# Optimization experiments

Measured on AMD Instinct MI355X. Metric: run time of the kernel, lower is better.

Reference implementation:

```python
import jax, jax.numpy as jnp
import numpy as np
from jax.scipy.special import logsumexp

REG = 1.0
N_ITER = 50  # fixed Sinkhorn iterations (log-domain, stabilized)


def setup_inputs() -> dict:
    key = jax.random.key(0)
    k1, k2 = jax.random.split(key)
    source = jax.random.normal(k1, (8192, 256), dtype=jnp.float32)
    target = jax.random.normal(k2, (8192, 256), dtype=jnp.float32)
    return {"source": source, "target": target}


def _sinkhorn_value(x, y, reg):
    # squared euclidean cost matrix [n, m]
    M = (jnp.sum(x * x, axis=1)[:, None]
         + jnp.sum(y * y, axis=1)[None, :]
         - 2.0 * (x @ y.T))
    n, m = M.shape
    loga = -jnp.log(jnp.float32(n))  # uniform weights
    logb = -jnp.log(jnp.float32(m))
    Mr = M / reg

    def step(fg, _):
        f, g = fg
        # f_i = -reg * logsumexp_j((g_j - M_ij)/reg + log b_j)
        f = -reg * logsumexp(g[None, :] / reg - Mr + logb, axis=1)
        g = -reg * logsumexp(f[:, None] / reg - Mr + loga, axis=0)
        return (f, g), None

    f0 = jnp.zeros((n,), dtype=M.dtype)
    g0 = jnp.zeros((m,), dtype=M.dtype)
    (f, g), _ = jax.lax.scan(step, (f0, g0), None, length=N_ITER)

    # log P_ij = (f_i + g_j - M_ij)/reg + log a_i + log b_j
    logP = (f[:, None] + g[None, :]) / reg - Mr + (loga + logb)
    P = jnp.exp(logP)
    value_linear = jnp.sum(P * M)
    # KL(P || a x b) entropic term (reg_type='KL' default in POT)
    kl = jnp.sum(P * (logP - loga - logb))
    return value_linear + reg * kl


def reference(source, target):
    value = _sinkhorn_value(source, target, REG)
    return jnp.sqrt(value)
```

## Files before the change

### kernel.cpp

```cpp
#include <hip/hip_runtime.h>

#define N 8192
#define DK 256
#define LOG2E 1.4426950408889634f
#define LN2   0.6931471805599453f
#define ZS    2.5f
#define QS    1.1541560327f
#define BIAS  320.0f

typedef unsigned short u16;
typedef u16   ushort8 __attribute__((ext_vector_type(8)));
typedef __bf16 bf16x8 __attribute__((ext_vector_type(8)));
typedef float  f32x4  __attribute__((ext_vector_type(4)));

__device__ __forceinline__ u16 f2bf(float f){
  unsigned u = __builtin_bit_cast(unsigned, f);
  return (u16)((u + 0x7fffu + ((u >> 16) & 1u)) >> 16);
}
__device__ __forceinline__ float ex2(float x){
  float r; asm("v_exp_f32 %0, %1" : "=v"(r) : "v"(x)); return r;
}
__device__ __forceinline__ float lg2(float x){
  float r; asm("v_log_f32 %0, %1" : "=v"(r) : "v"(x)); return r;
}
__device__ __forceinline__ float cub0(unsigned u){ float r; asm("v_cvt_f32_ubyte0 %0, %1":"=v"(r):"v"(u)); return r; }
__device__ __forceinline__ float cub1(unsigned u){ float r; asm("v_cvt_f32_ubyte1 %0, %1":"=v"(r):"v"(u)); return r; }
__device__ __forceinline__ float cub2(unsigned u){ float r; asm("v_cvt_f32_ubyte2 %0, %1":"=v"(r):"v"(u)); return r; }
__device__ __forceinline__ float cub3(unsigned u){ float r; asm("v_cvt_f32_ubyte3 %0, %1":"=v"(r):"v"(u)); return r; }

__device__ __forceinline__ float quad(unsigned u, float4 gv, float M){
  float t0 = __builtin_fmaf(cub0(u), ZS, gv.x - M);
  float t1 = __builtin_fmaf(cub1(u), ZS, gv.y - M);
  float t2 = __builtin_fmaf(cub2(u), ZS, gv.z - M);
  float t3 = __builtin_fmaf(cub3(u), ZS, gv.w - M);
  return (ex2(t0) + ex2(t1)) + (ex2(t2) + ex2(t3));
}
__device__ __forceinline__ void upd16(const uint4 a, const float* gp, float& m, float& s){
  const float4 g0 = *(const float4*)(gp);
  const float4 g1 = *(const float4*)(gp + 4);
  const float4 g2 = *(const float4*)(gp + 8);
  const float4 g3 = *(const float4*)(gp + 12);
  float t0  = __builtin_fmaf(cub0(a.x), ZS, g0.x);
  float t1  = __builtin_fmaf(cub1(a.x), ZS, g0.y);
  float t2  = __builtin_fmaf(cub2(a.x), ZS, g0.z);
  float t3  = __builtin_fmaf(cub3(a.x), ZS, g0.w);
  float t4  = __builtin_fmaf(cub0(a.y), ZS, g1.x);
  float t5  = __builtin_fmaf(cub1(a.y), ZS, g1.y);
  float t6  = __builtin_fmaf(cub2(a.y), ZS, g1.z);
  float t7  = __builtin_fmaf(cub3(a.y), ZS, g1.w);
  float t8  = __builtin_fmaf(cub0(a.z), ZS, g2.x);
  float t9  = __builtin_fmaf(cub1(a.z), ZS, g2.y);
  float t10 = __builtin_fmaf(cub2(a.z), ZS, g2.z);
  float t11 = __builtin_fmaf(cub3(a.z), ZS, g2.w);
  float t12 = __builtin_fmaf(cub0(a.w), ZS, g3.x);
  float t13 = __builtin_fmaf(cub1(a.w), ZS, g3.y);
  float t14 = __builtin_fmaf(cub2(a.w), ZS, g3.z);
  float t15 = __builtin_fmaf(cub3(a.w), ZS, g3.w);
  float a0 = fmaxf(t0, t1),   a1 = fmaxf(t2, t3);
  float a2 = fmaxf(t4, t5),   a3 = fmaxf(t6, t7);
  float a4 = fmaxf(t8, t9),   a5 = fmaxf(t10, t11);
  float a6 = fmaxf(t12, t13), a7 = fmaxf(t14, t15);
  float b0 = fmaxf(a0, a1), b1 = fmaxf(a2, a3), b2 = fmaxf(a4, a5), b3 = fmaxf(a6, a7);
  float nm = fmaxf(fmaxf(fmaxf(b0, b1), fmaxf(b2, b3)), m);
  float s0 = ex2(t0 - nm) + ex2(t1 - nm) + ex2(t2 - nm) + ex2(t3 - nm)
           + ex2(t4 - nm) + ex2(t5 - nm) + ex2(t6 - nm) + ex2(t7 - nm);
  float s1 = ex2(t8 - nm) + ex2(t9 - nm) + ex2(t10 - nm) + ex2(t11 - nm)
           + ex2(t12 - nm) + ex2(t13 - nm) + ex2(t14 - nm) + ex2(t15 - nm);
  s = __builtin_fmaf(s, ex2(m - nm), s0 + s1);
  m = nm;
}

__global__ __launch_bounds__(256) void prep_k(const float* __restrict__ x, const float* __restrict__ y,
                                              u16* __restrict__ xb, u16* __restrict__ yb,
                                              float* __restrict__ x2, float* __restrict__ y2,
                                              float* __restrict__ gts){
  const int w = threadIdx.x >> 6, l = threadIdx.x & 63;
  const int r = blockIdx.x * 4 + w;
  const bool isx = r < N;
  const int rr = isx ? r : r - N;
  const float* src = (isx ? x : y) + (size_t)rr * DK;
  float4 v = *(const float4*)(src + l * 4);
  ushort4 bv;
  bv.x = f2bf(v.x); bv.y = f2bf(v.y); bv.z = f2bf(v.z); bv.w = f2bf(v.w);
  *(ushort4*)((isx ? xb : yb) + (size_t)rr * DK + l * 4) = bv;
  float p = v.x*v.x + v.y*v.y + v.z*v.z + v.w*v.w;
  #pragma unroll
  for (int off = 32; off > 0; off >>= 1) p += __shfl_down(p, off);
  if (l == 0){
    if (isx) x2[rr] = p;
    else { y2[rr] = p; gts[rr] = -p * LOG2E - BIAS; }
  }
}

__global__ __launch_bounds__(256) void gemm_k(const u16* __restrict__ xb, const u16* __restrict__ yb,
                                              unsigned char* __restrict__ zq,
                                              unsigned char* __restrict__ zqT){
  __shared__ __align__(16) u16 As[128 * 72];
  __shared__ __align__(16) u16 Bs[128 * 72];
  const int t = threadIdx.x;
  const int w = t >> 6, l = t & 63;
  const int wm = w >> 1, wn = w & 1;
  const int brow = blockIdx.y * 128, bcol = blockIdx.x * 128;
  const int tr = t >> 3, tc = t & 7;
  f32x4 acc[4][4] = {};
  for (int ks = 0; ks < 4; ++ks){
    #pragma unroll
    for (int rr = 0; rr < 4; ++rr){
      const int row = tr + rr * 32;
      *(ushort8*)&As[row * 72 + tc * 8] = *(const ushort8*)&xb[(size_t)(brow + row) * DK + ks * 64 + tc * 8];
      *(ushort8*)&Bs[row * 72 + tc * 8] = *(const ushort8*)&yb[(size_t)(bcol + row) * DK + ks * 64 + tc * 8];
    }
    __syncthreads();
    #pragma unroll
    for (int kk = 0; kk < 2; ++kk){
      bf16x8 av[4], bv[4];
      #pragma unroll
      for (int mi = 0; mi < 4; ++mi){
        const int ar = wm * 64 + mi * 16 + (l & 15);
        av[mi] = __builtin_bit_cast(bf16x8, *(const ushort8*)&As[ar * 72 + kk * 32 + (l >> 4) * 8]);
      }
      #pragma unroll
      for (int ni = 0; ni < 4; ++ni){
        const int br = wn * 64 + ni * 16 + (l & 15);
        bv[ni] = __builtin_bit_cast(bf16x8, *(const ushort8*)&Bs[br * 72 + kk * 32 + (l >> 4) * 8]);
      }
      #pragma unroll
      for (int mi = 0; mi < 4; ++mi)
        #pragma unroll
        for (int ni = 0; ni < 4; ++ni)
          acc[mi][ni] = __builtin_amdgcn_mfma_f32_16x16x32_bf16(av[mi], bv[ni], acc[mi][ni], 0, 0, 0);
    }
    __syncthreads();
  }
  unsigned char* Cs = (unsigned char*)As;
  unsigned char* Ct = (unsigned char*)Bs;
  #pragma unroll
  for (int mi = 0; mi < 4; ++mi){
    const int rowb = wm * 64 + mi * 16 + (l >> 4) * 4;
    #pragma unroll
    for (int ni = 0; ni < 4; ++ni){
      const int col = wn * 64 + ni * 16 + (l & 15);
      unsigned pk = 0;
      #pragma unroll
      for (int rr = 0; rr < 4; ++rr){
        float q = fminf(fmaxf(acc[mi][ni][rr] * QS, -127.f), 127.f);
        unsigned b = (unsigned)((int)__builtin_rintf(q) + 128) & 255u;
        Cs[(rowb + rr) * 128 + col] = (unsigned char)b;
        pk |= b << (8 * rr);
      }
      *(unsigned*)(Ct + col * 144 + rowb) = pk;
    }
  }
  __syncthreads();
  const int trow0 = t >> 3, kseg = t & 7;
  #pragma unroll
  for (int ii = 0; ii < 4; ++ii){
    const int row = trow0 + ii * 32;
    int4 v = *(const int4*)(Cs + row * 128 + kseg * 16);
    *(int4*)(zq + (size_t)(brow + row) * N + bcol + kseg * 16) = v;
    int4 vt = *(const int4*)(Ct + row * 144 + kseg * 16);
    *(int4*)(zqT + (size_t)(bcol + row) * N + brow + kseg * 16) = vt;
  }
}

__global__ __launch_bounds__(256) void sweept_k(const unsigned char* __restrict__ z,
                                                const float* __restrict__ din,
                                                float* __restrict__ dout,
                                                float* __restrict__ pmax_out){
  const int w = threadIdx.x >> 6, l = threadIdx.x & 63;
  const int i = blockIdx.x * 4 + w;
  const unsigned char* zr = z + (size_t)i * N + l * 16;
  float m = -1e30f, s = 0.f;
  #pragma unroll 2
  for (int it = 0; it < 8; ++it){
    const uint4 zA = *(const uint4*)(zr + it * 1024);
    upd16(zA, din + it * 1024 + l * 16, m, s);
  }
  #pragma unroll
  for (int off = 32; off > 0; off >>= 1){
    float om = __shfl_down(m, off);
    float os = __shfl_down(s, off);
    float nm = fmaxf(m, om);
    s = __builtin_fmaf(s, ex2(m - nm), os * ex2(om - nm));
    m = nm;
  }
  if (l == 0){
    float lse2 = m + lg2(s);
    dout[i] = 13.0f - lse2 - BIAS;
    pmax_out[i] = lse2;
  }
}

template<int MODE>
__global__ __launch_bounds__(256) void sweepf_k(const unsigned char* __restrict__ z,
                                                const float* __restrict__ din,
                                                float* __restrict__ dout,
                                                const float* __restrict__ pmax_in,
                                                float* __restrict__ pmax_out,
                                                const float* __restrict__ fprev,
                                                const float* __restrict__ x2,
                                                float* __restrict__ contrib){
  const int w = threadIdx.x >> 6, l = threadIdx.x & 63;
  const int r0 = blockIdx.x * 16 + w * 4;
  const unsigned char* zr = z + (size_t)r0 * N + l * 16;
  const float M0 = pmax_in[r0],     M1 = pmax_in[r0 + 1];
  const float M2 = pmax_in[r0 + 2], M3 = pmax_in[r0 + 3];
  float s0 = 0.f, s1 = 0.f, s2 = 0.f, s3 = 0.f;
  #pragma unroll
  for (int it = 0; it < 8; ++it){
    const uint4 a0 = *(const uint4*)(zr + it * 1024);
    const uint4 a1 = *(const uint4*)(zr + N + it * 1024);
    const uint4 a2 = *(const uint4*)(zr + 2 * N + it * 1024);
    const uint4 a3 = *(const uint4*)(zr + 3 * N + it * 1024);
    const float* gp = din + it * 1024 + l * 16;
    const float4 g0 = *(const float4*)(gp);
    const float4 g1 = *(const float4*)(gp + 4);
    const float4 g2 = *(const float4*)(gp + 8);
    const float4 g3 = *(const float4*)(gp + 12);
    s0 += (quad(a0.x, g0, M0) + quad(a0.y, g1, M0))
        + (quad(a0.z, g2, M0) + quad(a0.w, g3, M0));
    s1 += (quad(a1.x, g0, M1) + quad(a1.y, g1, M1))
        + (quad(a1.z, g2, M1) + quad(a1.w, g3, M1));
    s2 += (quad(a2.x, g0, M2) + quad(a2.y, g1, M2))
        + (quad(a2.z, g2, M2) + quad(a2.w, g3, M2));
    s3 += (quad(a3.x, g0, M3) + quad(a3.y, g1, M3))
        + (quad(a3.z, g2, M3) + quad(a3.w, g3, M3));
  }
  #pragma unroll
  for (int off = 32; off > 0; off >>= 1){
    s0 += __shfl_down(s0, off);
    s1 += __shfl_down(s1, off);
    s2 += __shfl_down(s2, off);
    s3 += __shfl_down(s3, off);
  }
  if (l == 0){
    const float lse0 = M0 + lg2(s0);
    const float lse1 = M1 + lg2(s1);
    const float lse2 = M2 + lg2(s2);
    const float lse3 = M3 + lg2(s3);
    if (MODE == 0){
      dout[r0]     = 13.0f - lse0 - BIAS;
      dout[r0 + 1] = 13.0f - lse1 - BIAS;
      dout[r0 + 2] = 13.0f - lse2 - BIAS;
      dout[r0 + 3] = 13.0f - lse3 - BIAS;
      pmax_out[r0]     = lse0;
      pmax_out[r0 + 1] = lse1;
      pmax_out[r0 + 2] = lse2;
      pmax_out[r0 + 3] = lse3;
    } else {
      const float f0 = fprev[r0] + BIAS;
      const float f1 = fprev[r0 + 1] + BIAS;
      const float f2 = fprev[r0 + 2] + BIAS;
      const float f3 = fprev[r0 + 3] + BIAS;
      contrib[r0]     = (f0 * LN2 + x2[r0])     * ex2(f0 + lse0 - 26.0f);
      contrib[r0 + 1] = (f1 * LN2 + x2[r0 + 1]) * ex2(f1 + lse1 - 26.0f);
      contrib[r0 + 2] = (f2 * LN2 + x2[r0 + 2]) * ex2(f2 + lse2 - 26.0f);
      contrib[r0 + 3] = (f3 * LN2 + x2[r0 + 3]) * ex2(f3 + lse3 - 26.0f);
    }
  }
}

__global__ __launch_bounds__(256) void finish_k(const float* __restrict__ contrib,
                                                const float* __restrict__ gts,
                                                const float* __restrict__ y2,
                                                float* __restrict__ out){
  __shared__ float s1[256], s2[256];
  const int t = threadIdx.x;
  float a = 0.f, b = 0.f;
  for (int j = t; j < N; j += 256){ a += contrib[j]; b += (gts[j] + BIAS) * LN2 + y2[j]; }
  s1[t] = a; s2[t] = b; __syncthreads();
  for (int st = 128; st > 0; st >>= 1){
    if (t < st){ s1[t] += s1[t + st]; s2[t] += s2[t + st]; }
    __syncthreads();
  }
  if (t == 0) out[0] = sqrtf(s1[0] + s2[0] * (1.0f / (float)N));
}

extern "C" void kernel_launch(void* const* d_in, const int* in_sizes, int n_in,
                              void* d_out, int out_size, void* d_ws, size_t ws_size,
                              hipStream_t stream){
  const float* x = (const float*)d_in[0];
  const float* y = (const float*)d_in[1];
  float* out = (float*)d_out;
  char* ws = (char*)d_ws;

  unsigned char* zq  = (unsigned char*)(ws);
  unsigned char* zqT = (unsigned char*)(ws + 67108864);
  u16*   xb      = (u16*)  (ws + 134217728);
  u16*   yb      = (u16*)  (ws + 138412032);
  float* x2      = (float*)(ws + 142606336);
  float* y2      = (float*)(ws + 142639104);
  float* fts     = (float*)(ws + 142671872);
  float* gts     = (float*)(ws + 142704640);
  float* contrib = (float*)(ws + 142737408);
  float* pmaxF   = (float*)(ws + 142770176);
  float* pmaxG   = (float*)(ws + 142802944);

  prep_k<<<4096, 256, 0, stream>>>(x, y, xb, yb, x2, y2, gts);
  gemm_k<<<dim3(64, 64), 256, 0, stream>>>(xb, yb, zq, zqT);
  for (int it = 0; it < 2; ++it){
    sweept_k<<<2048, 256, 0, stream>>>(zq,  gts, fts, pmaxF);
    sweept_k<<<2048, 256, 0, stream>>>(zqT, fts, gts, pmaxG);
  }
  for (int s = 4; s < 100; ++s){
    if ((s & 1) == 0)
      sweepf_k<0><<<512, 256, 0, stream>>>(zq,  gts, fts, pmaxF, pmaxF,
                                           nullptr, nullptr, nullptr);
    else
      sweepf_k<0><<<512, 256, 0, stream>>>(zqT, fts, gts, pmaxG, pmaxG,
                                           nullptr, nullptr, nullptr);
  }
  sweepf_k<1><<<512, 256, 0, stream>>>(zq, gts, nullptr, pmaxF, nullptr,
                                       fts, x2, contrib);
  finish_k<<<1, 256, 0, stream>>>(contrib, gts, y2, out);
}
```

Baseline: 1.827 ms.

## Split sweep rows across four waves and raise grid to 2048 blocks

The fixed-max sweep kernel now gives each block 4 rows, with the 4 waves each covering a quarter of the columns, instead of each wave owning 4 full rows. Partial sums are combined through shared memory, and the grid grows from 512 to 2048 blocks. A launch-bounds occupancy hint is also added. The aim is more waves in flight on the MI355X's many CUs, to hide memory latency on the byte-quantized cost matrix. The cost is an extra block barrier and a shared-memory reduction per block.

```diff
diff --git a/kernel.cpp b/kernel.cpp
--- a/kernel.cpp
+++ b/kernel.cpp
@@ -34,6 +34,11 @@
   float t2 = __builtin_fmaf(cub2(u), ZS, gv.z - M);
   float t3 = __builtin_fmaf(cub3(u), ZS, gv.w - M);
   return (ex2(t0) + ex2(t1)) + (ex2(t2) + ex2(t3));
+}
+__device__ __forceinline__ float pm16(const uint4 a, const float4 g0, const float4 g1,
+                                      const float4 g2, const float4 g3, float M){
+  return (quad(a.x, g0, M) + quad(a.y, g1, M))
+       + (quad(a.z, g2, M) + quad(a.w, g3, M));
 }
 __device__ __forceinline__ void upd16(const uint4 a, const float* gp, float& m, float& s){
   const float4 g0 = *(const float4*)(gp);
@@ -192,39 +197,37 @@
 }
 
 template<int MODE>
-__global__ __launch_bounds__(256) void sweepf_k(const unsigned char* __restrict__ z,
-                                                const float* __restrict__ din,
-                                                float* __restrict__ dout,
-                                                const float* __restrict__ pmax_in,
-                                                float* __restrict__ pmax_out,
-                                                const float* __restrict__ fprev,
-                                                const float* __restrict__ x2,
-                                                float* __restrict__ contrib){
+__global__ __launch_bounds__(256, 6) void sweepf_k(const unsigned char* __restrict__ z,
+                                                   const float* __restrict__ din,
+                                                   float* __restrict__ dout,
+                                                   const float* __restrict__ pmax_in,
+                                                   float* __restrict__ pmax_out,
+                                                   const float* __restrict__ fprev,
+                                                   const float* __restrict__ x2,
+                                                   float* __restrict__ contrib){
+  __shared__ float sB[4][4];
   const int w = threadIdx.x >> 6, l = threadIdx.x & 63;
-  const int r0 = blockIdx.x * 16 + w * 4;
-  const unsigned char* zr = z + (size_t)r0 * N + l * 16;
+  const int r0 = blockIdx.x * 4;
+  const int cbase = w * 2048 + l * 16;
+  const unsigned char* zr = z + (size_t)r0 * N + cbase;
   const float M0 = pmax_in[r0],     M1 = pmax_in[r0 + 1];
   const float M2 = pmax_in[r0 + 2], M3 = pmax_in[r0 + 3];
   float s0 = 0.f, s1 = 0.f, s2 = 0.f, s3 = 0.f;
   #pragma unroll
-  for (int it = 0; it < 8; ++it){
+  for (int it = 0; it < 2; ++it){
     const uint4 a0 = *(const uint4*)(zr + it * 1024);
     const uint4 a1 = *(const uint4*)(zr + N + it * 1024);
     const uint4 a2 = *(const uint4*)(zr + 2 * N + it * 1024);
     const uint4 a3 = *(const uint4*)(zr + 3 * N + it * 1024);
-    const float* gp = din + it * 1024 + l * 16;
+    const float* gp = din + cbase + it * 1024;
     const float4 g0 = *(const float4*)(gp);
     const float4 g1 = *(const float4*)(gp + 4);
     const float4 g2 = *(const float4*)(gp + 8);
     const float4 g3 = *(const float4*)(gp + 12);
-    s0 += (quad(a0.x, g0, M0) + quad(a0.y, g1, M0))
-        + (quad(a0.z, g2, M0) + quad(a0.w, g3, M0));
-    s1 += (quad(a1.x, g0, M1) + quad(a1.y, g1, M1))
-        + (quad(a1.z, g2, M1) + quad(a1.w, g3, M1));
-    s2 += (quad(a2.x, g0, M2) + quad(a2.y, g1, M2))
-        + (quad(a2.z, g2, M2) + quad(a2.w, g3, M2));
-    s3 += (quad(a3.x, g0, M3) + quad(a3.y, g1, M3))
-        + (quad(a3.z, g2, M3) + quad(a3.w, g3, M3));
+    s0 += pm16(a0, g0, g1, g2, g3, M0);
+    s1 += pm16(a1, g0, g1, g2, g3, M1);
+    s2 += pm16(a2, g0, g1, g2, g3, M2);
+    s3 += pm16(a3, g0, g1, g2, g3, M3);
   }
   #pragma unroll
   for (int off = 32; off > 0; off >>= 1){
@@ -234,28 +237,21 @@
     s3 += __shfl_down(s3, off);
   }
   if (l == 0){
-    const float lse0 = M0 + lg2(s0);
-    const float lse1 = M1 + lg2(s1);
-    const float lse2 = M2 + lg2(s2);
-    const float lse3 = M3 + lg2(s3);
+    sB[w][0] = s0; sB[w][1] = s1; sB[w][2] = s2; sB[w][3] = s3;
+  }
+  __syncthreads();
+  if (threadIdx.x < 4){
+    const int j = threadIdx.x;
+    const int row = r0 + j;
+    const float s = (sB[0][j] + sB[1][j]) + (sB[2][j] + sB[3][j]);
+    const float M = pmax_in[row];
+    const float lse = M + lg2(s);
     if (MODE == 0){
-      dout[r0]     = 13.0f - lse0 - BIAS;
-      dout[r0 + 1] = 13.0f - lse1 - BIAS;
-      dout[r0 + 2] = 13.0f - lse2 - BIAS;
-      dout[r0 + 3] = 13.0f - lse3 - BIAS;
-      pmax_out[r0]     = lse0;
-      pmax_out[r0 + 1] = lse1;
-      pmax_out[r0 + 2] = lse2;
-      pmax_out[r0 + 3] = lse3;
+      dout[row] = 13.0f - lse - BIAS;
+      pmax_out[row] = lse;
     } else {
-      const float f0 = fprev[r0] + BIAS;
-      const float f1 = fprev[r0 + 1] + BIAS;
-      const float f2 = fprev[r0 + 2] + BIAS;
-      const float f3 = fprev[r0 + 3] + BIAS;
-      contrib[r0]     = (f0 * LN2 + x2[r0])     * ex2(f0 + lse0 - 26.0f);
-      contrib[r0 + 1] = (f1 * LN2 + x2[r0 + 1]) * ex2(f1 + lse1 - 26.0f);
-      contrib[r0 + 2] = (f2 * LN2 + x2[r0 + 2]) * ex2(f2 + lse2 - 26.0f);
-      contrib[r0 + 3] = (f3 * LN2 + x2[r0 + 3]) * ex2(f3 + lse3 - 26.0f);
+      const float f = fprev[row] + BIAS;
+      contrib[row] = (f * LN2 + x2[row]) * ex2(f + lse - 26.0f);
     }
   }
 }
@@ -304,13 +300,13 @@
   }
   for (int s = 4; s < 100; ++s){
     if ((s & 1) == 0)
-      sweepf_k<0><<<512, 256, 0, stream>>>(zq,  gts, fts, pmaxF, pmaxF,
-                                           nullptr, nullptr, nullptr);
+      sweepf_k<0><<<2048, 256, 0, stream>>>(zq,  gts, fts, pmaxF, pmaxF,
+                                            nullptr, nullptr, nullptr);
     else
-      sweepf_k<0><<<512, 256, 0, stream>>>(zqT, fts, gts, pmaxG, pmaxG,
-                                           nullptr, nullptr, nullptr);
-  }
-  sweepf_k<1><<<512, 256, 0, stream>>>(zq, gts, nullptr, pmaxF, nullptr,
-                                       fts, x2, contrib);
+      sweepf_k<0><<<2048, 256, 0, stream>>>(zqT, fts, gts, pmaxG, pmaxG,
+                                            nullptr, nullptr, nullptr);
+  }
+  sweepf_k<1><<<2048, 256, 0, stream>>>(zq, gts, nullptr, pmaxF, nullptr,
+                                        fts, x2, contrib);
   finish_k<<<1, 256, 0, stream>>>(contrib, gts, y2, out);
 }
```

Result: slower. 3.679 ms (+101.3%).
